# Kernel tuning notes

Measured on AMD Instinct MI355X. Metric: run time of the kernel, lower is better.

## Reference

```python
import jax, jax.numpy as jnp
import numpy as np

N, F, H, C = 16384, 512, 16, 16

def setup_inputs() -> dict:
    key = jax.random.key(0)
    ks = jax.random.split(key, 8)
    x = jax.random.normal(ks[0], (N, F), dtype=jnp.float32)
    adjacency = jax.random.uniform(ks[1], (N, N), dtype=jnp.float32)
    W1 = jax.random.normal(ks[2], (F, H), dtype=jnp.float32) * (1.0 / np.sqrt(F))
    b1 = jnp.zeros((H,), dtype=jnp.float32)
    W2 = jax.random.normal(ks[3], (H, C), dtype=jnp.float32) * (1.0 / np.sqrt(H))
    b2 = jnp.zeros((C,), dtype=jnp.float32)
    Wd = jax.random.normal(ks[4], (C, 1), dtype=jnp.float32) * (1.0 / np.sqrt(C))
    bd = jnp.zeros((1,), dtype=jnp.float32)
    return {"x": x, "adjacency": adjacency, "W1": W1, "b1": b1,
            "W2": W2, "b2": b2, "Wd": Wd, "bd": bd}

def reference(x, adjacency, W1, b1, W2, b2, Wd, bd):
    # GCN layer 1: relu(A @ (X @ W1) + b1)   -- [N,F]@[F,16] then [N,N]@[N,16]
    h = jax.nn.relu(adjacency @ (x @ W1) + b1)
    # dropout is a no-op at inference (training=False)
    # GCN layer 2: softmax(A @ (h @ W2) + b2) over classes
    h = jax.nn.softmax(adjacency @ (h @ W2) + b2, axis=-1)
    # dense head: linear activation -> [N, 1]
    out = h @ Wd + bd
    return out
```

## Files before the change

kernel.cpp:

```cpp
#include <hip/hip_runtime.h>
#include <hip/hip_bf16.h>

#define N_NODES 16384
#define FDIM 512

typedef __attribute__((address_space(1))) const void gvoid_t;
typedef __attribute__((address_space(3))) void lvoid_t;
typedef float vfloat4 __attribute__((ext_vector_type(4)));

#define SCHED_FENCE() __builtin_amdgcn_sched_barrier(0)

template <int KTOT, int RELU, int HASBIAS>
__global__ __launch_bounds__(256, 2)
void k_rowagg(const float* __restrict__ A,
              const float* __restrict__ V,
              const float* __restrict__ bias,
              float* __restrict__ out) {
    constexpr int KT = 256;
    constexpr int NT = KTOT / KT;
    constexpr int TB = KT * 16 * 4;
    __shared__ char lv[2 * TB];

    const int tid = threadIdx.x;
    const int lane = tid & 63;
    const int w = tid >> 6;
    const size_t row0 = (size_t)blockIdx.x * 16 + (size_t)w * 4;

    int sw_src[4];
#pragma unroll
    for (int s = 0; s < 4; ++s) {
        const int D = s * 4096 + tid * 16;
        sw_src[s] = (D ^ (((D >> 8) & 7) << 4)) >> 2;
    }

    unsigned zoff = 0;

    auto STAGE = [&](int halfoff, int t) {
        const float* vt = V + (size_t)t * (KT * 16);
#pragma unroll
        for (int s = 0; s < 4; ++s) {
            __builtin_amdgcn_global_load_lds(
                (gvoid_t*)(const void*)(vt + sw_src[s]),
                (lvoid_t*)(void*)(lv + zoff + halfoff + s * 4096 + tid * 16),
                16, 0, 0);
        }
    };

    auto LOADA = [&](vfloat4 (&a)[4], int t) {
#pragma unroll
        for (int r = 0; r < 4; ++r)
            a[r] = __builtin_nontemporal_load(
                reinterpret_cast<const vfloat4*>(
                    A + (row0 + r) * (size_t)KTOT + (size_t)t * KT + lane * 4));
    };

    float acc[4][16];
#pragma unroll
    for (int r = 0; r < 4; ++r)
#pragma unroll
        for (int c = 0; c < 16; ++c) acc[r][c] = 0.f;

    auto COMPUTE = [&](const vfloat4 (&a)[4], unsigned roff) {
#pragma unroll
        for (int kk = 0; kk < 4; ++kk) {
            vfloat4 vv[4];
#pragma unroll
            for (int cc = 0; cc < 4; ++cc) {
                const unsigned B = (unsigned)lane * 256u + ((unsigned)kk << 6) +
                                   ((unsigned)cc << 4);
                const unsigned P = B ^ (((unsigned)lane & 7u) << 4);
                vv[cc] = *reinterpret_cast<const vfloat4*>(lv + roff + P);
            }
#pragma unroll
            for (int cc = 0; cc < 4; ++cc) {
#pragma unroll
                for (int r = 0; r < 4; ++r) {
                    const float ak = a[r][kk];
                    acc[r][cc * 4 + 0] += ak * vv[cc][0];
                    acc[r][cc * 4 + 1] += ak * vv[cc][1];
                    acc[r][cc * 4 + 2] += ak * vv[cc][2];
                    acc[r][cc * 4 + 3] += ak * vv[cc][3];
                }
            }
        }
    };

    vfloat4 a0[4], a1[4];

    STAGE(0, 0);
    SCHED_FENCE();
    LOADA(a0, 0);
    SCHED_FENCE();
    asm volatile("s_waitcnt vmcnt(4)" ::: "memory");
    __builtin_amdgcn_s_barrier();
    asm volatile("" : "+v"(zoff));
    SCHED_FENCE();

#pragma unroll 1
    for (int t = 0; t < NT; t += 2) {
        STAGE(TB, t + 1);
        SCHED_FENCE();
        LOADA(a1, t + 1);
        SCHED_FENCE();
        COMPUTE(a0, zoff + 0);
        SCHED_FENCE();
        asm volatile("s_waitcnt vmcnt(4)" ::: "memory");
        __builtin_amdgcn_s_barrier();
        asm volatile("" : "+v"(zoff));
        SCHED_FENCE();

        if (t + 2 < NT) {
            STAGE(0, t + 2);
            SCHED_FENCE();
            LOADA(a0, t + 2);
            SCHED_FENCE();
            COMPUTE(a1, zoff + TB);
            SCHED_FENCE();
            asm volatile("s_waitcnt vmcnt(4)" ::: "memory");
            __builtin_amdgcn_s_barrier();
            asm volatile("" : "+v"(zoff));
            SCHED_FENCE();
        } else {
            COMPUTE(a1, zoff + TB);
        }
    }

    float o = 0.f;
#pragma unroll
    for (int r = 0; r < 4; ++r) {
#pragma unroll
        for (int c = 0; c < 16; ++c) {
            float s = acc[r][c];
            s += __shfl_xor(s, 1);  s += __shfl_xor(s, 2);  s += __shfl_xor(s, 4);
            s += __shfl_xor(s, 8);  s += __shfl_xor(s, 16); s += __shfl_xor(s, 32);
            o = (r * 16 + c == lane) ? s : o;
        }
    }
    if (HASBIAS) o += bias[lane & 15];
    if (RELU) o = fmaxf(o, 0.f);
    out[row0 * 16 + lane] = o;
}

__global__ __launch_bounds__(256) void k3_hw(const float* __restrict__ h1,
                                             const float* __restrict__ W2,
                                             float* __restrict__ hw) {
    __shared__ float w2s[256];
    w2s[threadIdx.x] = W2[threadIdx.x];
    __syncthreads();
    const size_t r = (size_t)blockIdx.x * 256 + threadIdx.x;
    float h[16];
#pragma unroll
    for (int q = 0; q < 4; ++q) {
        float4 v = *reinterpret_cast<const float4*>(h1 + r * 16 + q * 4);
        h[q * 4 + 0] = v.x; h[q * 4 + 1] = v.y; h[q * 4 + 2] = v.z; h[q * 4 + 3] = v.w;
    }
#pragma unroll
    for (int q = 0; q < 4; ++q) {
        float4 o;
#pragma unroll
        for (int j = 0; j < 4; ++j) {
            const int c = q * 4 + j;
            float s = 0.f;
#pragma unroll
            for (int k = 0; k < 16; ++k) s += h[k] * w2s[k * 16 + c];
            (&o.x)[j] = s;
        }
        *reinterpret_cast<float4*>(hw + r * 16 + q * 4) = o;
    }
}

__global__ __launch_bounds__(256) void k5_head(const float* __restrict__ g,
                                               const float* __restrict__ Wd,
                                               const float* __restrict__ bd,
                                               float* __restrict__ out) {
    const size_t r = (size_t)blockIdx.x * 256 + threadIdx.x;
    float v[16];
#pragma unroll
    for (int q = 0; q < 4; ++q) {
        float4 t = *reinterpret_cast<const float4*>(g + r * 16 + q * 4);
        v[q * 4 + 0] = t.x; v[q * 4 + 1] = t.y; v[q * 4 + 2] = t.z; v[q * 4 + 3] = t.w;
    }
    float m = v[0];
#pragma unroll
    for (int c = 1; c < 16; ++c) m = fmaxf(m, v[c]);
    float se = 0.f, sd = 0.f;
#pragma unroll
    for (int c = 0; c < 16; ++c) {
        const float e = expf(v[c] - m);
        se += e;
        sd += e * Wd[c];
    }
    out[r] = sd / se + bd[0];
}

extern "C" void kernel_launch(void* const* d_in, const int* in_sizes, int n_in,
                              void* d_out, int out_size, void* d_ws, size_t ws_size,
                              hipStream_t stream) {
    const float* x  = (const float*)d_in[0];
    const float* A  = (const float*)d_in[1];
    const float* W1 = (const float*)d_in[2];
    const float* b1 = (const float*)d_in[3];
    const float* W2 = (const float*)d_in[4];
    const float* b2 = (const float*)d_in[5];
    const float* Wd = (const float*)d_in[6];
    const float* bd = (const float*)d_in[7];
    float* out = (float*)d_out;

    float* ws = (float*)d_ws;
    float* xw = ws;
    float* h1 = ws + 1 * N_NODES * 16;
    float* hw = ws + 2 * N_NODES * 16;
    float* gl = ws + 3 * N_NODES * 16;

    k_rowagg<FDIM, 0, 0><<<N_NODES / 16, 256, 0, stream>>>(x, W1, b1, xw);
    k_rowagg<N_NODES, 1, 1><<<N_NODES / 16, 256, 0, stream>>>(A, xw, b1, h1);
    k3_hw<<<N_NODES / 256, 256, 0, stream>>>(h1, W2, hw);
    k_rowagg<N_NODES, 0, 1><<<N_NODES / 16, 256, 0, stream>>>(A, hw, b2, gl);
    k5_head<<<N_NODES / 256, 256, 0, stream>>>(gl, Wd, bd, out);
}
```

Baseline: 460.8 us.

## Add triple-buffered A·V aggregation kernel with two rows per wave

```diff
diff --git a/kernel.cpp b/kernel.cpp
--- a/kernel.cpp
+++ b/kernel.cpp
@@ -141,6 +141,178 @@
     out[row0 * 16 + lane] = o;
 }
 
+template <int RELU, int HASBIAS>
+__global__ __launch_bounds__(256, 2)
+void k_rowagg2(const float* __restrict__ A,
+               const float* __restrict__ V,
+               const float* __restrict__ bias,
+               float* __restrict__ out) {
+    constexpr int SLOT = 16384;
+    __shared__ char lv[3 * SLOT];
+
+    const int tid = threadIdx.x;
+    const int lane = tid & 63;
+    const int w = tid >> 6;
+    const size_t row0 = (size_t)blockIdx.x * 8 + (size_t)w * 2;
+
+    int sw_src[4];
+#pragma unroll
+    for (int s = 0; s < 4; ++s) {
+        const int D = s * 4096 + tid * 16;
+        sw_src[s] = (D ^ (((D >> 8) & 7) << 4)) >> 2;
+    }
+
+    unsigned zoff = 0;
+
+    auto STAGE = [&](unsigned slotoff, int h) {
+        const float* vt = V + (size_t)h * 4096;
+#pragma unroll
+        for (int s = 0; s < 4; ++s) {
+            __builtin_amdgcn_global_load_lds(
+                (gvoid_t*)(const void*)(vt + sw_src[s]),
+                (lvoid_t*)(void*)(lv + zoff + slotoff + s * 4096 + tid * 16),
+                16, 0, 0);
+        }
+    };
+
+    auto PAIR = [&](vfloat4 (&a)[2][2], int p) {
+#pragma unroll
+        for (int r = 0; r < 2; ++r) {
+            const float* ap = A + (row0 + r) * (size_t)N_NODES + (size_t)p * 512 + lane * 4;
+            a[r][0] = __builtin_nontemporal_load(reinterpret_cast<const vfloat4*>(ap));
+            a[r][1] = __builtin_nontemporal_load(reinterpret_cast<const vfloat4*>(ap + 256));
+        }
+    };
+
+    float acc[2][16];
+#pragma unroll
+    for (int r = 0; r < 2; ++r)
+#pragma unroll
+        for (int c = 0; c < 16; ++c) acc[r][c] = 0.f;
+
+    auto COMP = [&](const vfloat4& x0, const vfloat4& x1, unsigned roff) {
+#pragma unroll
+        for (int kk = 0; kk < 4; ++kk) {
+            vfloat4 vv[4];
+#pragma unroll
+            for (int cc = 0; cc < 4; ++cc) {
+                const unsigned B = (unsigned)lane * 256u + ((unsigned)kk << 6) +
+                                   ((unsigned)cc << 4);
+                const unsigned P = B ^ (((unsigned)lane & 7u) << 4);
+                vv[cc] = *reinterpret_cast<const vfloat4*>(lv + zoff + roff + P);
+            }
+#pragma unroll
+            for (int cc = 0; cc < 4; ++cc) {
+                const float a0k = x0[kk], a1k = x1[kk];
+                acc[0][cc * 4 + 0] += a0k * vv[cc][0];
+                acc[0][cc * 4 + 1] += a0k * vv[cc][1];
+                acc[0][cc * 4 + 2] += a0k * vv[cc][2];
+                acc[0][cc * 4 + 3] += a0k * vv[cc][3];
+                acc[1][cc * 4 + 0] += a1k * vv[cc][0];
+                acc[1][cc * 4 + 1] += a1k * vv[cc][1];
+                acc[1][cc * 4 + 2] += a1k * vv[cc][2];
+                acc[1][cc * 4 + 3] += a1k * vv[cc][3];
+            }
+        }
+    };
+
+#define VMW(n) asm volatile("s_waitcnt vmcnt(" #n ")" ::: "memory")
+#define BARL() do { __builtin_amdgcn_s_barrier(); \
+                    asm volatile("" : "+v"(zoff)); SCHED_FENCE(); } while (0)
+
+    vfloat4 aA[2][2], aB[2][2];
+    unsigned o0 = 0, o1 = SLOT, o2 = 2 * SLOT;
+
+    STAGE(o0, 0);
+    STAGE(o1, 1);
+    SCHED_FENCE();
+    PAIR(aA, 0);
+    SCHED_FENCE();
+    VMW(8);
+
+#pragma unroll 1
+    for (int it = 0; it < 15; ++it) {
+        const int j = 4 * it;
+        BARL();
+        STAGE(o2, j + 2);
+        SCHED_FENCE();
+        PAIR(aB, 2 * it + 1);
+        SCHED_FENCE();
+        VMW(12);
+        SCHED_FENCE();
+        COMP(aA[0][0], aA[1][0], o0);
+        SCHED_FENCE();
+        BARL();
+        STAGE(o0, j + 3);
+        SCHED_FENCE();
+        VMW(12);
+        SCHED_FENCE();
+        COMP(aA[0][1], aA[1][1], o1);
+        SCHED_FENCE();
+        BARL();
+        STAGE(o1, j + 4);
+        SCHED_FENCE();
+        PAIR(aA, 2 * it + 2);
+        SCHED_FENCE();
+        VMW(12);
+        SCHED_FENCE();
+        COMP(aB[0][0], aB[1][0], o2);
+        SCHED_FENCE();
+        BARL();
+        STAGE(o2, j + 5);
+        SCHED_FENCE();
+        VMW(12);
+        SCHED_FENCE();
+        COMP(aB[0][1], aB[1][1], o0);
+        SCHED_FENCE();
+        const unsigned tr = o0; o0 = o1; o1 = o2; o2 = tr;
+    }
+
+    BARL();
+    STAGE(o2, 62);
+    SCHED_FENCE();
+    PAIR(aB, 31);
+    SCHED_FENCE();
+    VMW(12);
+    SCHED_FENCE();
+    COMP(aA[0][0], aA[1][0], o0);
+    SCHED_FENCE();
+    BARL();
+    STAGE(o0, 63);
+    SCHED_FENCE();
+    VMW(12);
+    SCHED_FENCE();
+    COMP(aA[0][1], aA[1][1], o1);
+    SCHED_FENCE();
+    BARL();
+    VMW(0);
+    SCHED_FENCE();
+    COMP(aB[0][0], aB[1][0], o2);
+    SCHED_FENCE();
+    BARL();
+    COMP(aB[0][1], aB[1][1], o0);
+
+#undef VMW
+#undef BARL
+
+    float o = 0.f;
+#pragma unroll
+    for (int r = 0; r < 2; ++r) {
+#pragma unroll
+        for (int c = 0; c < 16; ++c) {
+            float s = acc[r][c];
+            s += __shfl_xor(s, 1);  s += __shfl_xor(s, 2);  s += __shfl_xor(s, 4);
+            s += __shfl_xor(s, 8);  s += __shfl_xor(s, 16); s += __shfl_xor(s, 32);
+            o = (r * 16 + c == lane) ? s : o;
+        }
+    }
+    if (lane < 32) {
+        if (HASBIAS) o += bias[lane & 15];
+        if (RELU) o = fmaxf(o, 0.f);
+        out[row0 * 16 + lane] = o;
+    }
+}
+
 __global__ __launch_bounds__(256) void k3_hw(const float* __restrict__ h1,
                                              const float* __restrict__ W2,
                                              float* __restrict__ hw) {
@@ -213,8 +385,8 @@
     float* gl = ws + 3 * N_NODES * 16;
 
     k_rowagg<FDIM, 0, 0><<<N_NODES / 16, 256, 0, stream>>>(x, W1, b1, xw);
-    k_rowagg<N_NODES, 1, 1><<<N_NODES / 16, 256, 0, stream>>>(A, xw, b1, h1);
+    k_rowagg2<1, 1><<<N_NODES / 8, 256, 0, stream>>>(A, xw, b1, h1);
     k3_hw<<<N_NODES / 256, 256, 0, stream>>>(h1, W2, hw);
-    k_rowagg<N_NODES, 0, 1><<<N_NODES / 16, 256, 0, stream>>>(A, hw, b2, gl);
+    k_rowagg2<0, 1><<<N_NODES / 8, 256, 0, stream>>>(A, hw, b2, gl);
     k5_head<<<N_NODES / 256, 256, 0, stream>>>(gl, Wd, bd, out);
 }
```

After: 562.4 us. 22.1% more time.
